# Kernel tuning notes

Measured on AMD Instinct MI355X. Metric: run time of the kernel, lower is better.

## Reference

```python
import jax, jax.numpy as jnp
import numpy as np

INV_SQRT3 = 1.0 / np.sqrt(3.0)


def setup_inputs() -> dict:
    key = jax.random.key(0)
    ks = jax.random.split(key, 7)
    N = 100000
    M0, M1 = 128, 64  # multiplicities of 0e and 1o irreps in in1 / out
    data_in1 = jax.random.normal(ks[0], (N, M0 + 3 * M1), jnp.float32)  # [N, 320]
    data_in2 = jax.random.normal(ks[1], (N, 1 + 3), jnp.float32)        # [N, 4] = 1x0e + 1x1o
    # e3nn-style path weights, standard normal init (path_normalization='none')
    W00 = jax.random.normal(ks[2], (M0, 1, M0), jnp.float32)  # 0e x 0e -> 0e
    W01 = jax.random.normal(ks[3], (M0, 1, M1), jnp.float32)  # 0e x 1o -> 1o
    W10 = jax.random.normal(ks[4], (M1, 1, M1), jnp.float32)  # 1o x 0e -> 1o
    W11 = jax.random.normal(ks[5], (M1, 1, M0), jnp.float32)  # 1o x 1o -> 0e
    # fan_in of the scalar output slice = 128*1 (0e x 0e) + 64*1 (1o x 1o) = 192
    sqrt_k = 1.0 / np.sqrt(M0 + M1)
    bias = jax.random.uniform(ks[6], (M0,), jnp.float32, -sqrt_k, sqrt_k)
    return {"data_in1": data_in1, "data_in2": data_in2,
            "W00": W00, "W01": W01, "W10": W10, "W11": W11, "bias": bias}


def reference(data_in1, data_in2, W00, W01, W10, W11, bias):
    M0, M1 = W00.shape[0], W10.shape[0]
    N = data_in1.shape[0]
    s1 = data_in1[:, :M0]                      # [N, 128]  scalars 0e
    v1 = data_in1[:, M0:].reshape(N, M1, 3)    # [N, 64, 3] vectors 1o
    s2 = data_in2[:, :1]                       # [N, 1]    scalar attr
    v2 = data_in2[:, 1:].reshape(N, 1, 3)      # [N, 1, 3] vector attr
    # CG paths (component irrep-normalization, path_normalization='none'):
    # wigner-3j folded analytically; net per-path coefs are 1,1,1,1/sqrt(3)
    out0 = jnp.einsum('nu,nv,uvw->nw', s1, s2, W00)                       # 0e x 0e -> 0e
    out0 = out0 + INV_SQRT3 * jnp.einsum('nui,nvi,uvw->nw', v1, v2, W11)  # 1o x 1o -> 0e
    outv = jnp.einsum('nu,nvk,uvw->nwk', s1, v2, W01)                     # 0e x 1o -> 1o
    outv = outv + jnp.einsum('nuk,nv,uvw->nwk', v1, s2, W10)              # 1o x 0e -> 1o
    # indexed bias add: bias_idx selects the l=0 output slice [0:M0]
    out0 = out0 + bias
    return jnp.concatenate([out0, outv.reshape(N, M1 * 3)], axis=1)      # [N, 320]
```

## Files before the change

### kernel.cpp

```cpp
#include <hip/hip_runtime.h>

typedef __bf16 bf16_8 __attribute__((ext_vector_type(8)));
typedef float  f32x4  __attribute__((ext_vector_type(4)));
typedef float  f32x3  __attribute__((ext_vector_type(3), aligned(4)));

#define INV_SQRT3f 0.57735026918962576f


__global__ void tp_convert_weights(
    const float* __restrict__ W00, const float* __restrict__ W01,
    const float* __restrict__ W10, const float* __restrict__ W11,
    __bf16* __restrict__ ws)
{
    const int chunk = blockIdx.x * blockDim.x + threadIdx.x;
    bf16_8 v;
    if (chunk < 2048) {
        const int c = chunk >> 4, q = chunk & 15;
#pragma unroll
        for (int j = 0; j < 8; ++j) v[j] = (__bf16)W00[(q * 8 + j) * 128 + c];
        *(bf16_8*)(ws + chunk * 8) = v;
    } else if (chunk < 3072) {
        const int idx = chunk - 2048;
        const int c = idx >> 4, q = idx & 15;
#pragma unroll
        for (int j = 0; j < 8; ++j) v[j] = (__bf16)W01[(q * 8 + j) * 64 + c];
        *(bf16_8*)(ws + 16384 + idx * 8) = v;
    } else if (chunk < 4096) {
        const int idx = chunk - 3072;
        const int c = idx >> 3, q = idx & 7;
#pragma unroll
        for (int j = 0; j < 8; ++j) v[j] = (__bf16)W11[(q * 8 + j) * 128 + c];
        *(bf16_8*)(ws + 24576 + idx * 8) = v;
    } else if (chunk < 4608) {
        const int idx = chunk - 4096;
        const int c = idx >> 3, q = idx & 7;
#pragma unroll
        for (int j = 0; j < 8; ++j) v[j] = (__bf16)W10[(q * 8 + j) * 64 + c];
        *(bf16_8*)(ws + 32768 + idx * 8) = v;
    }
}

__global__ __launch_bounds__(256, 2) void tp_main_kernel(
    const float* __restrict__ din1, const float* __restrict__ din2,
    const __bf16* __restrict__ wsw, const float* __restrict__ bias,
    float* __restrict__ out, int N, int nstrips)
{
    const int tid  = threadIdx.x;
    const int wid  = (blockIdx.x << 2) + (tid >> 6);
    if (wid >= nstrips) return;

    const int lane = tid & 63;
    const int mh   = lane & 15;
    const int kq   = lane >> 4;

    int row = wid * 16 + mh;  if (row >= N) row = N - 1;
    const float* __restrict__ r1 = din1 + row * 320;
    const f32x4 d2 = *(const f32x4*)(din2 + row * 4);
    const float s2 = d2.x;

    const __bf16* __restrict__ w00 = wsw;
    const __bf16* __restrict__ w01 = wsw + 16384;
    const __bf16* __restrict__ w11 = wsw + 24576;
    const __bf16* __restrict__ w10 = wsw + 32768;

    f32x4 accA[8];
    f32x4 accV[3][4];
#pragma unroll
    for (int i = 0; i < 8; ++i) accA[i] = (f32x4)0.0f;
#pragma unroll
    for (int k = 0; k < 3; ++k)
#pragma unroll
        for (int i = 0; i < 4; ++i) accV[k][i] = (f32x4)0.0f;

#pragma unroll
    for (int s = 0; s < 4; ++s) {
        const int off = 32 * s + 8 * kq;
        f32x4 x0 = *(const f32x4*)(r1 + off);
        f32x4 x1 = *(const f32x4*)(r1 + off + 4);
        float xx[8] = {x0.x, x0.y, x0.z, x0.w, x1.x, x1.y, x1.z, x1.w};
        bf16_8 as2, av0, av1, av2;
#pragma unroll
        for (int j = 0; j < 8; ++j) {
            as2[j] = (__bf16)(s2   * xx[j]);
            av0[j] = (__bf16)(d2.y * xx[j]);
            av1[j] = (__bf16)(d2.z * xx[j]);
            av2[j] = (__bf16)(d2.w * xx[j]);
        }
        const int q = 4 * s + kq;
#pragma unroll
        for (int nt = 0; nt < 8; ++nt) {
            const int c = nt * 16 + mh;
            bf16_8 b = *(const bf16_8*)(w00 + (c * 16 + q) * 8);
            accA[nt] = __builtin_amdgcn_mfma_f32_16x16x32_bf16(as2, b, accA[nt], 0, 0, 0);
        }
#pragma unroll
        for (int nt = 0; nt < 4; ++nt) {
            const int c = nt * 16 + mh;
            bf16_8 b = *(const bf16_8*)(w01 + (c * 16 + q) * 8);
            accV[0][nt] = __builtin_amdgcn_mfma_f32_16x16x32_bf16(av0, b, accV[0][nt], 0, 0, 0);
            accV[1][nt] = __builtin_amdgcn_mfma_f32_16x16x32_bf16(av1, b, accV[1][nt], 0, 0, 0);
            accV[2][nt] = __builtin_amdgcn_mfma_f32_16x16x32_bf16(av2, b, accV[2][nt], 0, 0, 0);
        }
    }

#pragma unroll
    for (int s = 0; s < 2; ++s) {
        const int voff = 128 + 96 * s + 24 * kq;
        float b24[24];
#pragma unroll
        for (int qq = 0; qq < 6; ++qq) {
            f32x4 t4 = *(const f32x4*)(r1 + voff + 4 * qq);
            b24[4 * qq]     = t4.x; b24[4 * qq + 1] = t4.y;
            b24[4 * qq + 2] = t4.z; b24[4 * qq + 3] = t4.w;
        }
        bf16_8 at, ac0, ac1, ac2;
#pragma unroll
        for (int j = 0; j < 8; ++j) {
            const float e0 = b24[3 * j], e1 = b24[3 * j + 1], e2 = b24[3 * j + 2];
            at[j]  = (__bf16)(INV_SQRT3f * (e0 * d2.y + e1 * d2.z + e2 * d2.w));
            ac0[j] = (__bf16)(s2 * e0);
            ac1[j] = (__bf16)(s2 * e1);
            ac2[j] = (__bf16)(s2 * e2);
        }
        const int q = 4 * s + kq;
#pragma unroll
        for (int nt = 0; nt < 8; ++nt) {
            const int c = nt * 16 + mh;
            bf16_8 b = *(const bf16_8*)(w11 + (c * 8 + q) * 8);
            accA[nt] = __builtin_amdgcn_mfma_f32_16x16x32_bf16(at, b, accA[nt], 0, 0, 0);
        }
#pragma unroll
        for (int nt = 0; nt < 4; ++nt) {
            const int c = nt * 16 + mh;
            bf16_8 b = *(const bf16_8*)(w10 + (c * 8 + q) * 8);
            accV[0][nt] = __builtin_amdgcn_mfma_f32_16x16x32_bf16(ac0, b, accV[0][nt], 0, 0, 0);
            accV[1][nt] = __builtin_amdgcn_mfma_f32_16x16x32_bf16(ac1, b, accV[1][nt], 0, 0, 0);
            accV[2][nt] = __builtin_amdgcn_mfma_f32_16x16x32_bf16(ac2, b, accV[2][nt], 0, 0, 0);
        }
    }

    const int rowg0 = wid * 16 + 4 * kq;
#pragma unroll
    for (int nt = 0; nt < 8; ++nt) {
        const float bi = bias[nt * 16 + mh];
#pragma unroll
        for (int r = 0; r < 4; ++r) {
            const int rowg = rowg0 + r;
            if (rowg < N) out[rowg * 320 + nt * 16 + mh] = accA[nt][r] + bi;
        }
    }
#pragma unroll
    for (int r = 0; r < 4; ++r) {
        const int rowg = rowg0 + r;
        if (rowg < N) {
#pragma unroll
            for (int nt = 0; nt < 4; ++nt) {
                const int w = nt * 16 + mh;
                f32x3 o;
                o.x = accV[0][nt][r];
                o.y = accV[1][nt][r];
                o.z = accV[2][nt][r];
                *(f32x3*)(out + rowg * 320 + 128 + 3 * w) = o;
            }
        }
    }
}

extern "C" void kernel_launch(void* const* d_in, const int* in_sizes, int n_in,
                              void* d_out, int out_size, void* d_ws, size_t ws_size,
                              hipStream_t stream)
{
    const float* din1 = (const float*)d_in[0];
    const float* din2 = (const float*)d_in[1];
    const float* W00  = (const float*)d_in[2];
    const float* W01  = (const float*)d_in[3];
    const float* W10  = (const float*)d_in[4];
    const float* W11  = (const float*)d_in[5];
    const float* bias = (const float*)d_in[6];
    float* outp = (float*)d_out;
    __bf16* ws = (__bf16*)d_ws;

    const int N = in_sizes[0] / 320;
    const int nstrips = (N + 15) / 16;
    const int nblocks = (nstrips + 3) / 4;

    hipLaunchKernelGGL(tp_convert_weights, dim3(18), dim3(256), 0, stream,
                       W00, W01, W10, W11, ws);
    hipLaunchKernelGGL(tp_main_kernel, dim3(nblocks), dim3(256), 0, stream,
                       din1, din2, ws, bias, outp, N, nstrips);
}
```

Measured before the change: 293.1 us.

## Stage bf16 weights in XOR-swizzled LDS and use 512-thread blocks

Each block now copies the W00, W01 and W11 bf16 weight tiles (64 KB) into shared memory and reads them from LDS instead of global/L1. The weight layout is XOR-swizzled in the conversion kernel so LDS reads spread across banks. Blocks grow to 8 waves so each LDS copy is shared by more row strips. W10 is still read from global memory. The 64 KB of LDS per block limits occupancy, and each block pays for the copy plus a barrier.

```diff
diff --git a/kernel.cpp b/kernel.cpp
--- a/kernel.cpp
+++ b/kernel.cpp
@@ -18,19 +18,19 @@
         const int c = chunk >> 4, q = chunk & 15;
 #pragma unroll
         for (int j = 0; j < 8; ++j) v[j] = (__bf16)W00[(q * 8 + j) * 128 + c];
-        *(bf16_8*)(ws + chunk * 8) = v;
+        *(bf16_8*)(ws + (c * 16 + (q ^ (c & 15))) * 8) = v;
     } else if (chunk < 3072) {
         const int idx = chunk - 2048;
         const int c = idx >> 4, q = idx & 15;
 #pragma unroll
         for (int j = 0; j < 8; ++j) v[j] = (__bf16)W01[(q * 8 + j) * 64 + c];
-        *(bf16_8*)(ws + 16384 + idx * 8) = v;
+        *(bf16_8*)(ws + 16384 + (c * 16 + (q ^ (c & 15))) * 8) = v;
     } else if (chunk < 4096) {
         const int idx = chunk - 3072;
         const int c = idx >> 3, q = idx & 7;
 #pragma unroll
         for (int j = 0; j < 8; ++j) v[j] = (__bf16)W11[(q * 8 + j) * 128 + c];
-        *(bf16_8*)(ws + 24576 + idx * 8) = v;
+        *(bf16_8*)(ws + 24576 + (c * 8 + (q ^ (c & 7))) * 8) = v;
     } else if (chunk < 4608) {
         const int idx = chunk - 4096;
         const int c = idx >> 3, q = idx & 7;
@@ -40,127 +40,139 @@
     }
 }
 
-__global__ __launch_bounds__(256, 2) void tp_main_kernel(
+__global__ __launch_bounds__(512, 4) void tp_main_kernel(
     const float* __restrict__ din1, const float* __restrict__ din2,
     const __bf16* __restrict__ wsw, const float* __restrict__ bias,
     float* __restrict__ out, int N, int nstrips)
 {
-    const int tid  = threadIdx.x;
-    const int wid  = (blockIdx.x << 2) + (tid >> 6);
-    if (wid >= nstrips) return;
-
-    const int lane = tid & 63;
-    const int mh   = lane & 15;
-    const int kq   = lane >> 4;
-
-    int row = wid * 16 + mh;  if (row >= N) row = N - 1;
-    const float* __restrict__ r1 = din1 + row * 320;
-    const f32x4 d2 = *(const f32x4*)(din2 + row * 4);
-    const float s2 = d2.x;
-
-    const __bf16* __restrict__ w00 = wsw;
-    const __bf16* __restrict__ w01 = wsw + 16384;
-    const __bf16* __restrict__ w11 = wsw + 24576;
-    const __bf16* __restrict__ w10 = wsw + 32768;
-
-    f32x4 accA[8];
-    f32x4 accV[3][4];
-#pragma unroll
-    for (int i = 0; i < 8; ++i) accA[i] = (f32x4)0.0f;
-#pragma unroll
-    for (int k = 0; k < 3; ++k)
-#pragma unroll
-        for (int i = 0; i < 4; ++i) accV[k][i] = (f32x4)0.0f;
-
-#pragma unroll
-    for (int s = 0; s < 4; ++s) {
-        const int off = 32 * s + 8 * kq;
-        f32x4 x0 = *(const f32x4*)(r1 + off);
-        f32x4 x1 = *(const f32x4*)(r1 + off + 4);
-        float xx[8] = {x0.x, x0.y, x0.z, x0.w, x1.x, x1.y, x1.z, x1.w};
-        bf16_8 as2, av0, av1, av2;
-#pragma unroll
-        for (int j = 0; j < 8; ++j) {
-            as2[j] = (__bf16)(s2   * xx[j]);
-            av0[j] = (__bf16)(d2.y * xx[j]);
-            av1[j] = (__bf16)(d2.z * xx[j]);
-            av2[j] = (__bf16)(d2.w * xx[j]);
-        }
-        const int q = 4 * s + kq;
+    __shared__ __attribute__((aligned(16))) __bf16 smem[32768];
+    const __bf16* sw00 = smem;
+    const __bf16* sw01 = smem + 16384;
+    const __bf16* sw11 = smem + 24576;
+
+    const int tid = threadIdx.x;
+
+    {
+        f32x4* d = (f32x4*)smem;
+        const f32x4* s = (const f32x4*)wsw;
+#pragma unroll
+        for (int i = 0; i < 8; ++i)
+            d[tid + 512 * i] = s[tid + 512 * i];
+    }
+    __syncthreads();
+
+    const int wid = (blockIdx.x << 3) + (tid >> 6);
+    if (wid < nstrips) {
+        const int lane = tid & 63;
+        const int mh   = lane & 15;
+        const int kq   = lane >> 4;
+
+        int row = wid * 16 + mh;  if (row >= N) row = N - 1;
+        const float* __restrict__ r1 = din1 + row * 320;
+        const f32x4 d2 = *(const f32x4*)(din2 + row * 4);
+        const float s2 = d2.x;
+
+        const __bf16* __restrict__ w10g = wsw + 32768;
+
+        f32x4 accA[8];
+        f32x4 accV[3][4];
+#pragma unroll
+        for (int i = 0; i < 8; ++i) accA[i] = (f32x4)0.0f;
+#pragma unroll
+        for (int k = 0; k < 3; ++k)
+#pragma unroll
+            for (int i = 0; i < 4; ++i) accV[k][i] = (f32x4)0.0f;
+
+#pragma unroll
+        for (int s = 0; s < 4; ++s) {
+            const int off = 32 * s + 8 * kq;
+            f32x4 x0 = *(const f32x4*)(r1 + off);
+            f32x4 x1 = *(const f32x4*)(r1 + off + 4);
+            float xx[8] = {x0.x, x0.y, x0.z, x0.w, x1.x, x1.y, x1.z, x1.w};
+            bf16_8 as2, av0, av1, av2;
+#pragma unroll
+            for (int j = 0; j < 8; ++j) {
+                as2[j] = (__bf16)(s2   * xx[j]);
+                av0[j] = (__bf16)(d2.y * xx[j]);
+                av1[j] = (__bf16)(d2.z * xx[j]);
+                av2[j] = (__bf16)(d2.w * xx[j]);
+            }
+            const int q = 4 * s + kq;
+#pragma unroll
+            for (int nt = 0; nt < 8; ++nt) {
+                const int c = nt * 16 + mh;
+                bf16_8 b = *(const bf16_8*)(sw00 + (c * 16 + (q ^ mh)) * 8);
+                accA[nt] = __builtin_amdgcn_mfma_f32_16x16x32_bf16(as2, b, accA[nt], 0, 0, 0);
+            }
+#pragma unroll
+            for (int nt = 0; nt < 4; ++nt) {
+                const int c = nt * 16 + mh;
+                bf16_8 b = *(const bf16_8*)(sw01 + (c * 16 + (q ^ mh)) * 8);
+                accV[0][nt] = __builtin_amdgcn_mfma_f32_16x16x32_bf16(av0, b, accV[0][nt], 0, 0, 0);
+                accV[1][nt] = __builtin_amdgcn_mfma_f32_16x16x32_bf16(av1, b, accV[1][nt], 0, 0, 0);
+                accV[2][nt] = __builtin_amdgcn_mfma_f32_16x16x32_bf16(av2, b, accV[2][nt], 0, 0, 0);
+            }
+        }
+
+#pragma unroll
+        for (int s = 0; s < 2; ++s) {
+            const int voff = 128 + 96 * s + 24 * kq;
+            float b24[24];
+#pragma unroll
+            for (int qq = 0; qq < 6; ++qq) {
+                f32x4 t4 = *(const f32x4*)(r1 + voff + 4 * qq);
+                b24[4 * qq]     = t4.x; b24[4 * qq + 1] = t4.y;
+                b24[4 * qq + 2] = t4.z; b24[4 * qq + 3] = t4.w;
+            }
+            bf16_8 at, ac0, ac1, ac2;
+#pragma unroll
+            for (int j = 0; j < 8; ++j) {
+                const float e0 = b24[3 * j], e1 = b24[3 * j + 1], e2 = b24[3 * j + 2];
+                at[j]  = (__bf16)(INV_SQRT3f * (e0 * d2.y + e1 * d2.z + e2 * d2.w));
+                ac0[j] = (__bf16)(s2 * e0);
+                ac1[j] = (__bf16)(s2 * e1);
+                ac2[j] = (__bf16)(s2 * e2);
+            }
+            const int q = 4 * s + kq;
+#pragma unroll
+            for (int nt = 0; nt < 8; ++nt) {
+                const int c = nt * 16 + mh;
+                bf16_8 b = *(const bf16_8*)(sw11 + (c * 8 + (q ^ (mh & 7))) * 8);
+                accA[nt] = __builtin_amdgcn_mfma_f32_16x16x32_bf16(at, b, accA[nt], 0, 0, 0);
+            }
+#pragma unroll
+            for (int nt = 0; nt < 4; ++nt) {
+                const int c = nt * 16 + mh;
+                bf16_8 b = *(const bf16_8*)(w10g + (c * 8 + q) * 8);
+                accV[0][nt] = __builtin_amdgcn_mfma_f32_16x16x32_bf16(ac0, b, accV[0][nt], 0, 0, 0);
+                accV[1][nt] = __builtin_amdgcn_mfma_f32_16x16x32_bf16(ac1, b, accV[1][nt], 0, 0, 0);
+                accV[2][nt] = __builtin_amdgcn_mfma_f32_16x16x32_bf16(ac2, b, accV[2][nt], 0, 0, 0);
+            }
+        }
+
+        const int rowg0 = wid * 16 + 4 * kq;
 #pragma unroll
         for (int nt = 0; nt < 8; ++nt) {
-            const int c = nt * 16 + mh;
-            bf16_8 b = *(const bf16_8*)(w00 + (c * 16 + q) * 8);
-            accA[nt] = __builtin_amdgcn_mfma_f32_16x16x32_bf16(as2, b, accA[nt], 0, 0, 0);
-        }
-#pragma unroll
-        for (int nt = 0; nt < 4; ++nt) {
-            const int c = nt * 16 + mh;
-            bf16_8 b = *(const bf16_8*)(w01 + (c * 16 + q) * 8);
-            accV[0][nt] = __builtin_amdgcn_mfma_f32_16x16x32_bf16(av0, b, accV[0][nt], 0, 0, 0);
-            accV[1][nt] = __builtin_amdgcn_mfma_f32_16x16x32_bf16(av1, b, accV[1][nt], 0, 0, 0);
-            accV[2][nt] = __builtin_amdgcn_mfma_f32_16x16x32_bf16(av2, b, accV[2][nt], 0, 0, 0);
-        }
-    }
-
-#pragma unroll
-    for (int s = 0; s < 2; ++s) {
-        const int voff = 128 + 96 * s + 24 * kq;
-        float b24[24];
-#pragma unroll
-        for (int qq = 0; qq < 6; ++qq) {
-            f32x4 t4 = *(const f32x4*)(r1 + voff + 4 * qq);
-            b24[4 * qq]     = t4.x; b24[4 * qq + 1] = t4.y;
-            b24[4 * qq + 2] = t4.z; b24[4 * qq + 3] = t4.w;
-        }
-        bf16_8 at, ac0, ac1, ac2;
-#pragma unroll
-        for (int j = 0; j < 8; ++j) {
-            const float e0 = b24[3 * j], e1 = b24[3 * j + 1], e2 = b24[3 * j + 2];
-            at[j]  = (__bf16)(INV_SQRT3f * (e0 * d2.y + e1 * d2.z + e2 * d2.w));
-            ac0[j] = (__bf16)(s2 * e0);
-            ac1[j] = (__bf16)(s2 * e1);
-            ac2[j] = (__bf16)(s2 * e2);
-        }
-        const int q = 4 * s + kq;
-#pragma unroll
-        for (int nt = 0; nt < 8; ++nt) {
-            const int c = nt * 16 + mh;
-            bf16_8 b = *(const bf16_8*)(w11 + (c * 8 + q) * 8);
-            accA[nt] = __builtin_amdgcn_mfma_f32_16x16x32_bf16(at, b, accA[nt], 0, 0, 0);
-        }
-#pragma unroll
-        for (int nt = 0; nt < 4; ++nt) {
-            const int c = nt * 16 + mh;
-            bf16_8 b = *(const bf16_8*)(w10 + (c * 8 + q) * 8);
-            accV[0][nt] = __builtin_amdgcn_mfma_f32_16x16x32_bf16(ac0, b, accV[0][nt], 0, 0, 0);
-            accV[1][nt] = __builtin_amdgcn_mfma_f32_16x16x32_bf16(ac1, b, accV[1][nt], 0, 0, 0);
-            accV[2][nt] = __builtin_amdgcn_mfma_f32_16x16x32_bf16(ac2, b, accV[2][nt], 0, 0, 0);
-        }
-    }
-
-    const int rowg0 = wid * 16 + 4 * kq;
-#pragma unroll
-    for (int nt = 0; nt < 8; ++nt) {
-        const float bi = bias[nt * 16 + mh];
+            const float bi = bias[nt * 16 + mh];
+#pragma unroll
+            for (int r = 0; r < 4; ++r) {
+                const int rowg = rowg0 + r;
+                if (rowg < N) out[rowg * 320 + nt * 16 + mh] = accA[nt][r] + bi;
+            }
+        }
 #pragma unroll
         for (int r = 0; r < 4; ++r) {
             const int rowg = rowg0 + r;
-            if (rowg < N) out[rowg * 320 + nt * 16 + mh] = accA[nt][r] + bi;
-        }
-    }
-#pragma unroll
-    for (int r = 0; r < 4; ++r) {
-        const int rowg = rowg0 + r;
-        if (rowg < N) {
-#pragma unroll
-            for (int nt = 0; nt < 4; ++nt) {
-                const int w = nt * 16 + mh;
-                f32x3 o;
-                o.x = accV[0][nt][r];
-                o.y = accV[1][nt][r];
-                o.z = accV[2][nt][r];
-                *(f32x3*)(out + rowg * 320 + 128 + 3 * w) = o;
+            if (rowg < N) {
+#pragma unroll
+                for (int nt = 0; nt < 4; ++nt) {
+                    const int w = nt * 16 + mh;
+                    f32x3 o;
+                    o.x = accV[0][nt][r];
+                    o.y = accV[1][nt][r];
+                    o.z = accV[2][nt][r];
+                    *(f32x3*)(out + rowg * 320 + 128 + 3 * w) = o;
+                }
             }
         }
     }
@@ -182,10 +194,10 @@
 
     const int N = in_sizes[0] / 320;
     const int nstrips = (N + 15) / 16;
-    const int nblocks = (nstrips + 3) / 4;
+    const int nblocks = (nstrips + 7) / 8;
 
     hipLaunchKernelGGL(tp_convert_weights, dim3(18), dim3(256), 0, stream,
                        W00, W01, W10, W11, ws);
-    hipLaunchKernelGGL(tp_main_kernel, dim3(nblocks), dim3(256), 0, stream,
+    hipLaunchKernelGGL(tp_main_kernel, dim3(nblocks), dim3(512), 0, stream,
                        din1, din2, ws, bias, outp, N, nstrips);
 }
```

New measurement: 283.2 us. -3.4%, faster.
